# Kernel tuning notes

Hardware: AMD Instinct MI355X
Metric: run time of the kernel (lower is better)

## Reference

```python
import jax, jax.numpy as jnp
import numpy as np

DIM, N_HEADS, GROUPS = 1152, 8, 4
HEAD_DIM = DIM // N_HEADS            # 144
KV_HEADS = N_HEADS // GROUPS         # 2
BSZ, SEQLEN, MAX_SEQ = 4, 2048, 2048
BASE = 10000.0


def _rope(x, cos, sin):
    # x: (b, s, h, d); cos/sin: (s, d//2)
    b, s, h, d = x.shape
    xr = x.astype(jnp.float32).reshape(b, s, h, d // 2, 2)
    xe, xo = xr[..., 0], xr[..., 1]
    c = cos[None, :, None, :]
    sn = sin[None, :, None, :]
    yr = xe * c - xo * sn
    yi = xe * sn + xo * c
    return jnp.stack([yr, yi], axis=-1).reshape(b, s, h, d).astype(x.dtype)


def setup_inputs() -> dict:
    key = jax.random.key(0)
    ks = jax.random.split(key, 8)
    std = 1.0 / np.sqrt(DIM)
    x = jax.random.normal(ks[0], (BSZ, SEQLEN, DIM), jnp.float32)
    wq = jax.random.normal(ks[1], (DIM, DIM), jnp.float32) * std
    bq = jnp.zeros((DIM,), jnp.float32)
    wkv = jax.random.normal(ks[2], (2 * KV_HEADS * HEAD_DIM, DIM), jnp.float32) * std
    bkv = jnp.zeros((2 * KV_HEADS * HEAD_DIM,), jnp.float32)
    wo = jax.random.normal(ks[3], (DIM, DIM), jnp.float32) * std
    bo = jnp.zeros((DIM,), jnp.float32)
    # rotary freqs: (seqlen, head_dim//2)
    inv = 1.0 / (BASE ** (jnp.arange(0, HEAD_DIM, 2, dtype=jnp.float32) / HEAD_DIM))
    t = jnp.arange(SEQLEN, dtype=jnp.float32)
    ang = jnp.outer(t, inv)
    freqs_cos, freqs_sin = jnp.cos(ang), jnp.sin(ang)
    # causal mask (s, t)
    mask = jnp.where(jnp.tril(jnp.ones((SEQLEN, SEQLEN), bool)), 0.0, -1e9).astype(jnp.float32)
    k_cache = jnp.zeros((BSZ, MAX_SEQ, KV_HEADS, HEAD_DIM), jnp.float32)
    v_cache = jnp.zeros((BSZ, MAX_SEQ, KV_HEADS, HEAD_DIM), jnp.float32)
    return {"x": x, "wq": wq, "bq": bq, "wkv": wkv, "bkv": bkv, "wo": wo, "bo": bo,
            "freqs_cos": freqs_cos, "freqs_sin": freqs_sin,
            "k_cache": k_cache, "v_cache": v_cache, "mask": mask, "start_pos": 0}


def reference(x, wq, bq, wkv, bkv, wo, bo, freqs_cos, freqs_sin, k_cache, v_cache, mask, start_pos):
    b, s, _ = x.shape
    end_pos = start_pos + s
    q = (x @ wq.T + bq).reshape(b, s, N_HEADS, HEAD_DIM)
    kv = (x @ wkv.T + bkv).reshape(b, s, 2, KV_HEADS, HEAD_DIM)
    k, v = kv[:, :, 0], kv[:, :, 1]
    rq = _rope(q, freqs_cos, freqs_sin)
    rk = _rope(k, freqs_cos, freqs_sin)
    k_cache = jax.lax.dynamic_update_slice(k_cache, rk, (0, start_pos, 0, 0))
    v_cache = jax.lax.dynamic_update_slice(v_cache, v, (0, start_pos, 0, 0))
    keys = jnp.repeat(k_cache[:, :end_pos], GROUPS, axis=2)   # (b, t, H, d)
    vals = jnp.repeat(v_cache[:, :end_pos], GROUPS, axis=2)
    scale = HEAD_DIM ** -0.5
    attn = jnp.einsum('bshd,bthd->bsht', rq, keys) * scale
    attn = attn + mask[:, None, :]
    scores = jax.nn.softmax(attn.astype(jnp.float32), axis=-1).astype(x.dtype)
    out = jnp.einsum('bsht,bthd->bshd', scores, vals)
    return out.reshape(b, s, DIM) @ wo.T + bo
```

## Files before the change

### kernel.cpp

```cpp
#include <hip/hip_runtime.h>


#define THREADS 256

typedef _Float16 f16x8 __attribute__((ext_vector_type(8)));
typedef _Float16 f16x4 __attribute__((ext_vector_type(4)));
typedef _Float16 f16x2 __attribute__((ext_vector_type(2)));
typedef float f32x4 __attribute__((ext_vector_type(4)));

#define GLDS16(gp, lp)                                                  \
  __builtin_amdgcn_global_load_lds(                                     \
      (const __attribute__((address_space(1))) unsigned int*)(gp),      \
      (__attribute__((address_space(3))) unsigned int*)(lp), 16, 0, 0)

__global__ __launch_bounds__(THREADS) void cvt_sw(const float* __restrict__ in,
                                                  _Float16* __restrict__ out,
                                                  int nG, int KC, int nrows) {
  int i = blockIdx.x * THREADS + threadIdx.x;
  if (i >= nG) return;
  int rr = i & 127;
  int j = i >> 7;
  int kc = j % KC;
  int rb = j / KC;
  int R = rb * 128 + rr;
  if (R >= nrows) R = nrows - 1;
  const float* src = in + (size_t)R * (KC * 8) + kc * 8;
  float4 a = *(const float4*)src;
  float4 c = *(const float4*)(src + 4);
  f16x8 o;
  o[0] = (_Float16)a.x; o[1] = (_Float16)a.y;
  o[2] = (_Float16)a.z; o[3] = (_Float16)a.w;
  o[4] = (_Float16)c.x; o[5] = (_Float16)c.y;
  o[6] = (_Float16)c.z; o[7] = (_Float16)c.w;
  *(f16x8*)(out + (size_t)i * 8) = o;
}

__global__ __launch_bounds__(THREADS) void prep_bias(const float* __restrict__ bq,
                                                     const float* __restrict__ bkv,
                                                     float* __restrict__ bias) {
  int i = blockIdx.x * THREADS + threadIdx.x;
  if (i < 1152) bias[i] = bq[i];
  else if (i < 1728) bias[i] = bkv[i - 1152];
}

__global__ __launch_bounds__(THREADS) void gemm_sw(
    const _Float16* __restrict__ A, const _Float16* __restrict__ B,
    const float* __restrict__ bias, float* __restrict__ C, int M, int N, int K) {
  __shared__ __align__(16) _Float16 As[1024 * 8];
  __shared__ __align__(16) _Float16 Bs[1024 * 8];
  const int t = threadIdx.x;
  const int w = t >> 6, lane = t & 63;
  const int quad = lane >> 4, l16 = lane & 15;
  const int wm = (w & 1) << 6, wn = (w >> 1) << 6;
  const int KC = K >> 3;
  const int mb = blockIdx.y, nb = blockIdx.x;
  const int m0 = mb << 7, n0 = nb << 7;

  f32x4 acc[4][4] = {};

  for (int kcb = 0; kcb < KC; kcb += 8) {
    const size_t Ab = ((size_t)mb * KC + kcb) << 7;
    const size_t Bb = ((size_t)nb * KC + kcb) << 7;
#pragma unroll
    for (int j = 0; j < 4; ++j) {
      const int ii = (w << 2) + j;
      GLDS16(A + ((Ab + (ii << 6) + lane) << 3), &As[(ii << 6) * 8]);
      GLDS16(B + ((Bb + (ii << 6) + lane) << 3), &Bs[(ii << 6) * 8]);
    }
    __syncthreads();
#pragma unroll
    for (int ks = 0; ks < 2; ++ks) {
      f16x8 af[4], bf[4];
#pragma unroll
      for (int mi = 0; mi < 4; ++mi)
        af[mi] = *(const f16x8*)&As[((((ks << 2) + quad) << 7) + wm + (mi << 4) + l16) * 8];
#pragma unroll
      for (int ni = 0; ni < 4; ++ni)
        bf[ni] = *(const f16x8*)&Bs[((((ks << 2) + quad) << 7) + wn + (ni << 4) + l16) * 8];
#pragma unroll
      for (int mi = 0; mi < 4; ++mi)
#pragma unroll
        for (int ni = 0; ni < 4; ++ni)
          acc[mi][ni] =
              __builtin_amdgcn_mfma_f32_16x16x32_f16(af[mi], bf[ni], acc[mi][ni], 0, 0, 0);
    }
    __syncthreads();
  }

#pragma unroll
  for (int mi = 0; mi < 4; ++mi) {
    const int row = m0 + wm + (mi << 4) + (quad << 2);
#pragma unroll
    for (int ni = 0; ni < 4; ++ni) {
      const int col = n0 + wn + (ni << 4) + l16;
      if (col < N) {
        const float bv = bias[col];
#pragma unroll
        for (int r = 0; r < 4; ++r)
          C[(size_t)(row + r) * N + col] = acc[mi][ni][r] + bv;
      }
    }
  }
}

__global__ __launch_bounds__(THREADS) void rope_scatter_f16(
    const float* __restrict__ qkv, const float* __restrict__ fc,
    const float* __restrict__ fs, _Float16* __restrict__ Qh,
    _Float16* __restrict__ Ksw) {
  int idx = blockIdx.x * THREADS + threadIdx.x;
  int m = idx / 720;
  int c = idx - m * 720;
  int s = m & 2047, b = m >> 11;
  const float* row = qkv + (size_t)m * 1728;
  int h, d2;
  const float* src;
  _Float16* dst;
  if (c < 576) {
    h = c / 72;
    d2 = c - h * 72;
    src = row + h * 144 + 2 * d2;
    dst = Qh + ((size_t)(b * 8 + h) * 2048 + s) * 144 + 2 * d2;
  } else {
    int cc = c - 576;
    h = cc / 72;
    d2 = cc - h * 72;
    src = row + 1152 + h * 144 + 2 * d2;
    size_t g = ((size_t)(b * 2 + h) * 64 + (s >> 5)) * 576 + (d2 >> 2) * 32 + (s & 31);
    dst = Ksw + g * 8 + (d2 & 3) * 2;
  }
  float2 v = *(const float2*)src;
  float cth = fc[s * 72 + d2], sth = fs[s * 72 + d2];
  f16x2 o;
  o.x = (_Float16)(v.x * cth - v.y * sth);
  o.y = (_Float16)(v.x * sth + v.y * cth);
  *(f16x2*)dst = o;
}

__global__ __launch_bounds__(THREADS) void v_transpose(const float* __restrict__ qkv,
                                                       _Float16* __restrict__ Vsw) {
  __shared__ _Float16 tile[128 * 145];
  const int t = threadIdx.x;
  const int s0 = blockIdx.x * 128;
  const int kvh = blockIdx.y, b = blockIdx.z;
  const float* src = qkv + ((size_t)(b * 2048 + s0)) * 1728 + 1440 + kvh * 144;
#pragma unroll
  for (int i = 0; i < 18; ++i) {
    int c = t + i * 256;
    int r = c / 36, cc = c - r * 36;
    float4 v = *(const float4*)(src + (size_t)r * 1728 + cc * 4);
    int base = r * 145 + cc * 4;
    tile[base + 0] = (_Float16)v.x;
    tile[base + 1] = (_Float16)v.y;
    tile[base + 2] = (_Float16)v.z;
    tile[base + 3] = (_Float16)v.w;
  }
  __syncthreads();
  const size_t tb = ((size_t)(b * 2 + kvh) * 64 + (s0 >> 5)) * 576;
#pragma unroll
  for (int i = 0; i < 9; ++i) {
    int c = t + i * 256;
    int sc = c / 144, d = c - sc * 144;
    f16x8 o;
#pragma unroll
    for (int j = 0; j < 8; ++j) o[j] = tile[(sc * 8 + j) * 145 + d];
    size_t g = tb + (size_t)(sc >> 2) * 576 + (sc & 3) * 144 + d;
    *(f16x8*)(Vsw + g * 8) = o;
  }
}

#define STAGE_TILE(kt)                                                     \
  do {                                                                     \
    const _Float16* Kt_ = Ksw + (tbase + (size_t)(kt)) * 4608;             \
    const _Float16* Vt_ = Vsw + (tbase + (size_t)(kt)) * 4608;             \
    for (int c = w; c < 18; c += 8) {                                      \
      if (c < 9)                                                           \
        GLDS16(Kt_ + ((c << 6) + lane) * 8, &Ks[(c << 6) * 8]);            \
      else                                                                 \
        GLDS16(Vt_ + (((c - 9) << 6) + lane) * 8,                          \
               &Vs[((c - 9) << 6) * 8]);                                   \
    }                                                                      \
  } while (0)

__global__ __launch_bounds__(512, 4) void attn_mfma(
    const _Float16* __restrict__ Qh, const _Float16* __restrict__ Ksw,
    const _Float16* __restrict__ Vsw, _Float16* __restrict__ Out) {
  __shared__ __align__(16) _Float16 Ks[576 * 8];
  __shared__ __align__(16) _Float16 Vs[576 * 8];
  __shared__ __align__(16) _Float16 Ps[128 * 40];
  const int t = threadIdx.x;
  const int w = t >> 6, lane = t & 63;
  const int w4 = w & 3;
  const int quad = lane >> 4, l16 = lane & 15;
  const int x = blockIdx.x, hp = blockIdx.y, b = blockIdx.z;
  const int h = hp * 2 + (w >> 2);
  const int kvh = hp >> 1;
  const int qi = (b == 0) ? x
               : (b == 1) ? ((x + 16) & 31)
               : (b == 2) ? (31 - x)
                          : ((15 - x) & 31);
  const int q0 = qi * 64;
  const int nkt = 2 * qi + 2;
  const _Float16* Qg = Qh + ((size_t)(b * 8 + h) * 2048 + q0) * 144;
  const size_t tbase = (size_t)(b * 2 + kvh) * 64;

  f16x8 qf[4];
  f16x4 qt4;
  {
    const _Float16* qp = Qg + (size_t)(w4 * 16 + l16) * 144;
#pragma unroll
    for (int ks = 0; ks < 4; ++ks) qf[ks] = *(const f16x8*)(qp + ks * 32 + quad * 8);
    qt4 = *(const f16x4*)(qp + 128 + quad * 4);
  }

  f32x4 Oacc[9] = {};
  float mrow[4] = {-3e38f, -3e38f, -3e38f, -3e38f};
  float lrow[4] = {0.f, 0.f, 0.f, 0.f};
  const float scale = 0.08333333333333333f;
  const int colb = (l16 & ~1);
  const int rsel = (lane & 1) << 1;

  for (int kt = 0; kt < nkt; ++kt) {
    STAGE_TILE(kt);
    __syncthreads();

    f32x4 sc[2] = {};
#pragma unroll
    for (int ks = 0; ks < 4; ++ks) {
#pragma unroll
      for (int ct = 0; ct < 2; ++ct) {
        f16x8 bfr = *(const f16x8*)&Ks[(((ks * 4 + quad) << 5) + ct * 16 + l16) * 8];
        sc[ct] = __builtin_amdgcn_mfma_f32_16x16x32_f16(qf[ks], bfr, sc[ct], 0, 0, 0);
      }
    }
#pragma unroll
    for (int ct = 0; ct < 2; ++ct) {
      f16x4 bt = *(const f16x4*)&Ks[(((16 + (quad >> 1)) << 5) + ct * 16 + l16) * 8 +
                                    (quad & 1) * 4];
      sc[ct] = __builtin_amdgcn_mfma_f32_16x16x16f16(qt4, bt, sc[ct], 0, 0, 0);
    }

    const bool band = (kt >= nkt - 2);
    const int rowb = q0 + w4 * 16 + quad * 4;
    float vv[2][4];
    float mx[4] = {-3e38f, -3e38f, -3e38f, -3e38f};
#pragma unroll
    for (int ct = 0; ct < 2; ++ct) {
      const int cb = kt * 32 + ct * 16 + l16;
#pragma unroll
      for (int r = 0; r < 4; ++r) {
        float v = sc[ct][r] * scale;
        if (band && cb > rowb + r) v -= 1e9f;
        vv[ct][r] = v;
        mx[r] = fmaxf(mx[r], v);
      }
    }
    float alv[4];
#pragma unroll
    for (int r = 0; r < 4; ++r) {
      float m = mx[r];
      m = fmaxf(m, __shfl_xor(m, 1));
      m = fmaxf(m, __shfl_xor(m, 2));
      m = fmaxf(m, __shfl_xor(m, 4));
      m = fmaxf(m, __shfl_xor(m, 8));
      float mn = fmaxf(mrow[r], m);
      alv[r] = __expf(mrow[r] - mn);
      mrow[r] = mn;
    }
    float rs[4] = {0.f, 0.f, 0.f, 0.f};
#pragma unroll
    for (int ct = 0; ct < 2; ++ct) {
      float p[4], q[4];
#pragma unroll
      for (int r = 0; r < 4; ++r) {
        p[r] = __expf(vv[ct][r] - mrow[r]);
        rs[r] += p[r];
      }
#pragma unroll
      for (int r = 0; r < 4; ++r) q[r] = __shfl_xor(p[r], 1);
#pragma unroll
      for (int k = 0; k < 2; ++k) {
        const int r = rsel + k;
        f16x2 pv;
        if (lane & 1) {
          pv.x = (_Float16)q[r];
          pv.y = (_Float16)p[r];
        } else {
          pv.x = (_Float16)p[r];
          pv.y = (_Float16)q[r];
        }
        *(f16x2*)&Ps[(w * 16 + quad * 4 + r) * 40 + ct * 16 + colb] = pv;
      }
    }
#pragma unroll
    for (int r = 0; r < 4; ++r) {
      float v = rs[r];
      v += __shfl_xor(v, 1);
      v += __shfl_xor(v, 2);
      v += __shfl_xor(v, 4);
      v += __shfl_xor(v, 8);
      lrow[r] = lrow[r] * alv[r] + v;
    }
#pragma unroll
    for (int nt = 0; nt < 9; ++nt)
#pragma unroll
      for (int r = 0; r < 4; ++r) Oacc[nt][r] *= alv[r];

    {
      f16x8 pa = *(const f16x8*)&Ps[(w * 16 + l16) * 40 + quad * 8];
#pragma unroll
      for (int nt = 0; nt < 9; ++nt) {
        f16x8 vb = *(const f16x8*)&Vs[(quad * 144 + nt * 16 + l16) * 8];
        Oacc[nt] = __builtin_amdgcn_mfma_f32_16x16x32_f16(pa, vb, Oacc[nt], 0, 0, 0);
      }
    }
    __syncthreads();
  }

  float inv[4];
#pragma unroll
  for (int r = 0; r < 4; ++r) inv[r] = 1.f / lrow[r];
#pragma unroll
  for (int nt = 0; nt < 9; ++nt) {
    float o[4], qn[4];
#pragma unroll
    for (int r = 0; r < 4; ++r) o[r] = Oacc[nt][r] * inv[r];
#pragma unroll
    for (int r = 0; r < 4; ++r) qn[r] = __shfl_xor(o[r], 1);
#pragma unroll
    for (int k = 0; k < 2; ++k) {
      const int r = rsel + k;
      f16x2 pv;
      if (lane & 1) {
        pv.x = (_Float16)qn[r];
        pv.y = (_Float16)o[r];
      } else {
        pv.x = (_Float16)o[r];
        pv.y = (_Float16)qn[r];
      }
      const size_t grow = (size_t)b * 2048 + q0 + w4 * 16 + quad * 4 + r;
      const size_t g = ((grow >> 7) * 144 + h * 18 + nt * 2 + (colb >> 3)) * 128 +
                       (grow & 127);
      *(f16x2*)(Out + g * 8 + (colb & 7)) = pv;
    }
  }
}

extern "C" void kernel_launch(void* const* d_in, const int* in_sizes, int n_in,
                              void* d_out, int out_size, void* d_ws, size_t ws_size,
                              hipStream_t stream) {
  const float* x = (const float*)d_in[0];
  const float* wq = (const float*)d_in[1];
  const float* bq = (const float*)d_in[2];
  const float* wkv = (const float*)d_in[3];
  const float* bkv = (const float*)d_in[4];
  const float* wo = (const float*)d_in[5];
  const float* bo = (const float*)d_in[6];
  const float* fc = (const float*)d_in[7];
  const float* fs = (const float*)d_in[8];
  float* out = (float*)d_out;
  char* ws = (char*)d_ws;

  _Float16* x_sw = (_Float16*)(ws + 0);
  _Float16* wqkv_sw = (_Float16*)(ws + 18874368);
  _Float16* wo_sw = (_Float16*)(ws + 23003136);
  float* bias_qkv = (float*)(ws + 25657344);
  float* qkv = (float*)(ws + 25664256);
  _Float16* Qh = (_Float16*)(ws + 82287360);
  _Float16* Ksw = (_Float16*)(ws + 101161728);
  _Float16* Vsw = (_Float16*)(ws + 105880320);
  _Float16* attn_sw = (_Float16*)(ws + 110598912);

  cvt_sw<<<4608, THREADS, 0, stream>>>(x, x_sw, 1179648, 144, 8192);
  cvt_sw<<<648, THREADS, 0, stream>>>(wq, wqkv_sw, 165888, 144, 1152);
  cvt_sw<<<360, THREADS, 0, stream>>>(wkv, wqkv_sw + 1327104, 92160, 144, 576);
  cvt_sw<<<648, THREADS, 0, stream>>>(wo, wo_sw, 165888, 144, 1152);
  prep_bias<<<7, THREADS, 0, stream>>>(bq, bkv, bias_qkv);

  gemm_sw<<<dim3(14, 64), THREADS, 0, stream>>>(x_sw, wqkv_sw, bias_qkv, qkv,
                                                8192, 1728, 1152);

  rope_scatter_f16<<<23040, THREADS, 0, stream>>>(qkv, fc, fs, Qh, Ksw);
  v_transpose<<<dim3(16, 2, 4), THREADS, 0, stream>>>(qkv, Vsw);

  attn_mfma<<<dim3(32, 4, 4), 512, 0, stream>>>(Qh, Ksw, Vsw, attn_sw);

  gemm_sw<<<dim3(9, 64), THREADS, 0, stream>>>(attn_sw, wo_sw, bo, out, 8192,
                                               1152, 1152);
}
```

Baseline: 421.5 us.

## Double-buffer K/V tiles with register prefetch in attention kernel

Replaces the direct global-to-LDS loads of each K/V tile with a register-staged prefetch of the next tile, issued before the current tile's compute and written into a second LDS buffer afterward. This lets global-memory latency overlap the QK and PV MFMA work and removes one barrier per iteration. In exchange it doubles K/V shared memory, which may reduce occupancy at 4 blocks per CU, and adds registers holding the prefetched data.

```diff
diff --git a/kernel.cpp b/kernel.cpp
--- a/kernel.cpp
+++ b/kernel.cpp
@@ -168,24 +168,11 @@
   }
 }
 
-#define STAGE_TILE(kt)                                                     \
-  do {                                                                     \
-    const _Float16* Kt_ = Ksw + (tbase + (size_t)(kt)) * 4608;             \
-    const _Float16* Vt_ = Vsw + (tbase + (size_t)(kt)) * 4608;             \
-    for (int c = w; c < 18; c += 8) {                                      \
-      if (c < 9)                                                           \
-        GLDS16(Kt_ + ((c << 6) + lane) * 8, &Ks[(c << 6) * 8]);            \
-      else                                                                 \
-        GLDS16(Vt_ + (((c - 9) << 6) + lane) * 8,                          \
-               &Vs[((c - 9) << 6) * 8]);                                   \
-    }                                                                      \
-  } while (0)
-
 __global__ __launch_bounds__(512, 4) void attn_mfma(
     const _Float16* __restrict__ Qh, const _Float16* __restrict__ Ksw,
     const _Float16* __restrict__ Vsw, _Float16* __restrict__ Out) {
-  __shared__ __align__(16) _Float16 Ks[576 * 8];
-  __shared__ __align__(16) _Float16 Vs[576 * 8];
+  __shared__ __align__(16) _Float16 Ks[2][576 * 8];
+  __shared__ __align__(16) _Float16 Vs[2][576 * 8];
   __shared__ __align__(16) _Float16 Ps[128 * 40];
   const int t = threadIdx.x;
   const int w = t >> 6, lane = t & 63;
@@ -203,6 +190,26 @@
   const _Float16* Qg = Qh + ((size_t)(b * 8 + h) * 2048 + q0) * 144;
   const size_t tbase = (size_t)(b * 2 + kvh) * 64;
 
+  f16x8 r0{}, r1{}, r2{};
+  auto ld_tile = [&](int kt) {
+    const _Float16* Kt_ = Ksw + (tbase + (size_t)kt) * 4608;
+    const _Float16* Vt_ = Vsw + (tbase + (size_t)kt) * 4608;
+    r0 = *(const f16x8*)(Kt_ + ((w << 6) + lane) * 8);
+    if (w == 0)
+      r1 = *(const f16x8*)(Kt_ + ((8 << 6) + lane) * 8);
+    else
+      r1 = *(const f16x8*)(Vt_ + (((w - 1) << 6) + lane) * 8);
+    if (w < 2) r2 = *(const f16x8*)(Vt_ + (((w + 7) << 6) + lane) * 8);
+  };
+  auto st_tile = [&](int buf) {
+    *(f16x8*)&Ks[buf][((w << 6) + lane) * 8] = r0;
+    if (w == 0)
+      *(f16x8*)&Ks[buf][((8 << 6) + lane) * 8] = r1;
+    else
+      *(f16x8*)&Vs[buf][(((w - 1) << 6) + lane) * 8] = r1;
+    if (w < 2) *(f16x8*)&Vs[buf][(((w + 7) << 6) + lane) * 8] = r2;
+  };
+
   f16x8 qf[4];
   f16x4 qt4;
   {
@@ -219,23 +226,28 @@
   const int colb = (l16 & ~1);
   const int rsel = (lane & 1) << 1;
 
+  ld_tile(0);
+  st_tile(0);
+  __syncthreads();
+
   for (int kt = 0; kt < nkt; ++kt) {
-    STAGE_TILE(kt);
-    __syncthreads();
+    const int cur = kt & 1;
+    const bool pf = (kt + 1 < nkt);
+    if (pf) ld_tile(kt + 1);
 
     f32x4 sc[2] = {};
 #pragma unroll
     for (int ks = 0; ks < 4; ++ks) {
 #pragma unroll
       for (int ct = 0; ct < 2; ++ct) {
-        f16x8 bfr = *(const f16x8*)&Ks[(((ks * 4 + quad) << 5) + ct * 16 + l16) * 8];
+        f16x8 bfr = *(const f16x8*)&Ks[cur][(((ks * 4 + quad) << 5) + ct * 16 + l16) * 8];
         sc[ct] = __builtin_amdgcn_mfma_f32_16x16x32_f16(qf[ks], bfr, sc[ct], 0, 0, 0);
       }
     }
 #pragma unroll
     for (int ct = 0; ct < 2; ++ct) {
-      f16x4 bt = *(const f16x4*)&Ks[(((16 + (quad >> 1)) << 5) + ct * 16 + l16) * 8 +
-                                    (quad & 1) * 4];
+      f16x4 bt = *(const f16x4*)&Ks[cur][(((16 + (quad >> 1)) << 5) + ct * 16 + l16) * 8 +
+                                         (quad & 1) * 4];
       sc[ct] = __builtin_amdgcn_mfma_f32_16x16x16f16(qt4, bt, sc[ct], 0, 0, 0);
     }
 
@@ -309,10 +321,12 @@
       f16x8 pa = *(const f16x8*)&Ps[(w * 16 + l16) * 40 + quad * 8];
 #pragma unroll
       for (int nt = 0; nt < 9; ++nt) {
-        f16x8 vb = *(const f16x8*)&Vs[(quad * 144 + nt * 16 + l16) * 8];
+        f16x8 vb = *(const f16x8*)&Vs[cur][(quad * 144 + nt * 16 + l16) * 8];
         Oacc[nt] = __builtin_amdgcn_mfma_f32_16x16x32_f16(pa, vb, Oacc[nt], 0, 0, 0);
       }
     }
+
+    if (pf) st_tile(cur ^ 1);
     __syncthreads();
   }
 
```

After: 431.3 us. 2.3% more time.

## Split causal attention along KV into partial chunks and merge with a separate kernel

Applied to the files above, without the earlier changes.

Each query tile's KV range is split into chunks of up to 16 tiles, giving 80 blocks per (batch, head-pair) instead of 32. Every block writes an unnormalized partial output plus its row max and sum, and a new merge kernel combines them with log-sum-exp rescaling. The goal is to even out the causal load imbalance, since long rows no longer serialize on one block, and to raise occupancy. The cost is extra global traffic for the partials, an extra launch, and fp16 storage of the unnormalized partials. The partial buffers reuse the qkv workspace region, which is consumed before attention runs.

```diff
diff --git a/kernel.cpp b/kernel.cpp
--- a/kernel.cpp
+++ b/kernel.cpp
@@ -172,18 +172,19 @@
   do {                                                                     \
     const _Float16* Kt_ = Ksw + (tbase + (size_t)(kt)) * 4608;             \
     const _Float16* Vt_ = Vsw + (tbase + (size_t)(kt)) * 4608;             \
-    for (int c = w; c < 18; c += 8) {                                      \
-      if (c < 9)                                                           \
-        GLDS16(Kt_ + ((c << 6) + lane) * 8, &Ks[(c << 6) * 8]);            \
+    for (int cc_ = w; cc_ < 18; cc_ += 8) {                                \
+      if (cc_ < 9)                                                         \
+        GLDS16(Kt_ + ((cc_ << 6) + lane) * 8, &Ks[(cc_ << 6) * 8]);        \
       else                                                                 \
-        GLDS16(Vt_ + (((c - 9) << 6) + lane) * 8,                          \
-               &Vs[((c - 9) << 6) * 8]);                                   \
+        GLDS16(Vt_ + (((cc_ - 9) << 6) + lane) * 8,                        \
+               &Vs[((cc_ - 9) << 6) * 8]);                                 \
     }                                                                      \
   } while (0)
 
 __global__ __launch_bounds__(512, 4) void attn_mfma(
     const _Float16* __restrict__ Qh, const _Float16* __restrict__ Ksw,
-    const _Float16* __restrict__ Vsw, _Float16* __restrict__ Out) {
+    const _Float16* __restrict__ Vsw, _Float16* __restrict__ pO,
+    float* __restrict__ pml) {
   __shared__ __align__(16) _Float16 Ks[576 * 8];
   __shared__ __align__(16) _Float16 Vs[576 * 8];
   __shared__ __align__(16) _Float16 Ps[128 * 40];
@@ -194,12 +195,17 @@
   const int x = blockIdx.x, hp = blockIdx.y, b = blockIdx.z;
   const int h = hp * 2 + (w >> 2);
   const int kvh = hp >> 1;
-  const int qi = (b == 0) ? x
-               : (b == 1) ? ((x + 16) & 31)
-               : (b == 2) ? (31 - x)
-                          : ((15 - x) & 31);
+
+  int qi, c;
+  if (x < 8)       { qi = x;                 c = 0; }
+  else if (x < 24) { qi = 8 + ((x - 8) >> 1);  c = (x - 8) & 1; }
+  else if (x < 48) { qi = 16 + (x - 24) / 3;   c = (x - 24) % 3; }
+  else             { qi = 24 + ((x - 48) >> 2); c = (x - 48) & 3; }
+
   const int q0 = qi * 64;
   const int nkt = 2 * qi + 2;
+  const int k0 = c * 16;
+  const int kend = (k0 + 16 < nkt) ? k0 + 16 : nkt;
   const _Float16* Qg = Qh + ((size_t)(b * 8 + h) * 2048 + q0) * 144;
   const size_t tbase = (size_t)(b * 2 + kvh) * 64;
 
@@ -219,7 +225,7 @@
   const int colb = (l16 & ~1);
   const int rsel = (lane & 1) << 1;
 
-  for (int kt = 0; kt < nkt; ++kt) {
+  for (int kt = k0; kt < kend; ++kt) {
     STAGE_TILE(kt);
     __syncthreads();
 
@@ -316,33 +322,62 @@
     __syncthreads();
   }
 
-  float inv[4];
-#pragma unroll
-  for (int r = 0; r < 4; ++r) inv[r] = 1.f / lrow[r];
-#pragma unroll
-  for (int nt = 0; nt < 9; ++nt) {
-    float o[4], qn[4];
-#pragma unroll
-    for (int r = 0; r < 4; ++r) o[r] = Oacc[nt][r] * inv[r];
-#pragma unroll
-    for (int r = 0; r < 4; ++r) qn[r] = __shfl_xor(o[r], 1);
-#pragma unroll
-    for (int k = 0; k < 2; ++k) {
-      const int r = rsel + k;
-      f16x2 pv;
-      if (lane & 1) {
-        pv.x = (_Float16)qn[r];
-        pv.y = (_Float16)o[r];
-      } else {
-        pv.x = (_Float16)o[r];
-        pv.y = (_Float16)qn[r];
-      }
-      const size_t grow = (size_t)b * 2048 + q0 + w4 * 16 + quad * 4 + r;
-      const size_t g = ((grow >> 7) * 144 + h * 18 + nt * 2 + (colb >> 3)) * 128 +
-                       (grow & 127);
-      *(f16x2*)(Out + g * 8 + (colb & 7)) = pv;
-    }
-  }
+  const int pid = (b * 4 + hp) * 80 + x;
+  const int hsel = w >> 2;
+  _Float16* po = pO + ((size_t)pid * 2 + hsel) * 64 * 144;
+#pragma unroll
+  for (int nt = 0; nt < 9; ++nt)
+#pragma unroll
+    for (int r = 0; r < 4; ++r)
+      po[(w4 * 16 + quad * 4 + r) * 144 + nt * 16 + l16] = (_Float16)Oacc[nt][r];
+  if (l16 == 0) {
+    float* pm = pml + ((size_t)pid * 2 + hsel) * 128;
+#pragma unroll
+    for (int r = 0; r < 4; ++r) {
+      pm[(w4 * 16 + quad * 4 + r) * 2 + 0] = mrow[r];
+      pm[(w4 * 16 + quad * 4 + r) * 2 + 1] = lrow[r];
+    }
+  }
+}
+
+__global__ __launch_bounds__(128) void merge_partials(
+    const _Float16* __restrict__ pO, const float* __restrict__ pml,
+    _Float16* __restrict__ Out) {
+  const int j = blockIdx.x, rg = blockIdx.y, h = blockIdx.z;
+  const int t = threadIdx.x;
+  const int grow = rg * 128 + t;
+  const int b = grow >> 11, s = grow & 2047;
+  const int qi = s >> 6, r = s & 63;
+  const int hp = h >> 1, hs = h & 1;
+  int base, nc;
+  if (qi < 8)       { base = qi;                nc = 1; }
+  else if (qi < 16) { base = 8 + 2 * (qi - 8);  nc = 2; }
+  else if (qi < 24) { base = 24 + 3 * (qi - 16); nc = 3; }
+  else              { base = 48 + 4 * (qi - 24); nc = 4; }
+  const int pb = (b * 4 + hp) * 80 + base;
+
+  float m[4], l[4];
+  float M = -3e38f;
+  for (int i = 0; i < nc; ++i) {
+    const float* p = pml + ((size_t)(pb + i) * 2 + hs) * 128 + r * 2;
+    m[i] = p[0];
+    l[i] = p[1];
+    M = fmaxf(M, m[i]);
+  }
+  float acc[8] = {};
+  float L = 0.f;
+  for (int i = 0; i < nc; ++i) {
+    const float sc = __expf(m[i] - M);
+    L += sc * l[i];
+    f16x8 o = *(const f16x8*)(pO + (((size_t)(pb + i) * 2 + hs) * 64 + r) * 144 + j * 8);
+#pragma unroll
+    for (int e = 0; e < 8; ++e) acc[e] += sc * (float)o[e];
+  }
+  const float invL = 1.f / L;
+  f16x8 out;
+#pragma unroll
+  for (int e = 0; e < 8; ++e) out[e] = (_Float16)(acc[e] * invL);
+  *(f16x8*)(Out + (((size_t)(grow >> 7) * 144 + h * 18 + j) * 128 + (grow & 127)) * 8) = out;
 }
 
 extern "C" void kernel_launch(void* const* d_in, const int* in_sizes, int n_in,
@@ -365,6 +400,8 @@
   _Float16* wo_sw = (_Float16*)(ws + 23003136);
   float* bias_qkv = (float*)(ws + 25657344);
   float* qkv = (float*)(ws + 25664256);
+  _Float16* part_O = (_Float16*)(ws + 25664256);
+  float* part_ml = (float*)(ws + 72850176);
   _Float16* Qh = (_Float16*)(ws + 82287360);
   _Float16* Ksw = (_Float16*)(ws + 101161728);
   _Float16* Vsw = (_Float16*)(ws + 105880320);
@@ -382,7 +419,8 @@
   rope_scatter_f16<<<23040, THREADS, 0, stream>>>(qkv, fc, fs, Qh, Ksw);
   v_transpose<<<dim3(16, 2, 4), THREADS, 0, stream>>>(qkv, Vsw);
 
-  attn_mfma<<<dim3(32, 4, 4), 512, 0, stream>>>(Qh, Ksw, Vsw, attn_sw);
+  attn_mfma<<<dim3(80, 4, 4), 512, 0, stream>>>(Qh, Ksw, Vsw, part_O, part_ml);
+  merge_partials<<<dim3(18, 64, 8), 128, 0, stream>>>(part_O, part_ml, attn_sw);
 
   gemm_sw<<<dim3(9, 64), THREADS, 0, stream>>>(attn_sw, wo_sw, bo, out, 8192,
                                                1152, 1152);
```

New measurement: 453.3 us. 7.5% more time.
